# Kernel optimization log

Hardware: AMD Instinct MI355X
Metric: run time of the kernel (lower is better)

Reference implementation:

```python
import jax, jax.numpy as jnp
import numpy as np

TAU = 0.9
TOPK = 8
NUM_LAYERS = 3


def _layer_norm(x, g, b, eps=1e-5):
    mu = jnp.mean(x, axis=-1, keepdims=True)
    var = jnp.var(x, axis=-1, keepdims=True)
    return (x - mu) / jnp.sqrt(var + eps) * g + b


def _forward(x, edge_index, Wi, bi, wp, Wa, ba, ln1_g, ln1_b, ln2_g, ln2_b,
             W1, b1, W2, b2, Wc, bc, Wo, bo):
    N = x.shape[0]
    H = Wi.shape[1]
    # input projection + relu
    x = jax.nn.relu(x @ Wi + bi)
    src, dst = edge_index[0], edge_index[1]
    # ---- priority pi (computed under no_grad, dummy_alpha = 1, x_prev = 0) ----
    delta_x = jnp.sum(jnp.abs(x), axis=1)                      # [N]
    neigh = jax.ops.segment_sum(delta_x[src], dst, num_segments=N)
    pi = jax.lax.stop_gradient(jax.nn.sigmoid(x @ wp + neigh))  # [N]
    # ---- add self loops (selected subgraph == full graph) ----
    loops = jnp.arange(N, dtype=src.dtype)
    src_e = jnp.concatenate([src, loops])
    dst_e = jnp.concatenate([dst, loops])
    Et = src_e.shape[0]
    # ---- edge attention logits: att_mlp(cat[h_i, h_j, p_j]) computed as split matvec ----
    a_dst = x @ Wa[:H]          # contribution of h_i = x[dst]
    a_src = x @ Wa[H:2 * H]     # contribution of h_j = x[src]
    e = a_dst[dst_e] + a_src[src_e] + pi[src_e] * Wa[2 * H] + ba[0]
    e = jax.nn.leaky_relu(e, 0.2) / TAU
    e = jnp.clip(e, -5.0, 5.0)
    exp_e = jnp.exp(e)
    denom = jax.ops.segment_sum(exp_e, dst_e, num_segments=N)
    alpha = exp_e / (denom[dst_e] + 1e-16)
    # ---- per-destination top-k sparsification + renormalization (vectorized) ----
    order = jnp.lexsort((-alpha, dst_e))       # sort by dst, then alpha descending
    dst_s = dst_e[order]
    alpha_s = alpha[order]
    pos = jnp.arange(Et)
    is_new = jnp.concatenate([jnp.ones((1,), bool), dst_s[1:] != dst_s[:-1]])
    grp_start = jax.lax.cummax(jnp.where(is_new, pos, 0))
    rank = pos - grp_start                     # rank within each dst group
    keep = rank < TOPK
    ksum = jax.ops.segment_sum(jnp.where(keep, alpha_s, 0.0), dst_s, num_segments=N)
    alpha_new_s = jnp.where(keep, alpha_s / (ksum[dst_s] + 1e-16), 0.0)
    alpha = jnp.zeros((Et,), x.dtype).at[order].set(alpha_new_s)
    # ---- prenorm blocks with priority-weighted conv (dropout = identity, eval) ----
    h = x
    for l in range(NUM_LAYERS):
        hn = _layer_norm(h, ln1_g[l], ln1_b[l])
        xp = hn @ Wc[l] + bc[l]                               # conv linear
        msg = xp[src_e] * alpha[:, None]                      # [Et, H]
        agg = jax.ops.segment_sum(msg, dst_e, num_segments=N)  # scatter-add
        h = h + jax.nn.relu(agg)
        h2 = _layer_norm(h, ln2_g[l], ln2_b[l])
        h2 = jax.nn.gelu(h2 @ W1[l] + b1[l], approximate=False) @ W2[l] + b2[l]
        h = h + h2
    return h @ Wo + bo


def setup_inputs() -> dict:
    key = jax.random.key(0)
    ks = jax.random.split(key, 10)
    N, E, IN, H, OUT, L, F = 50000, 400000, 256, 256, 64, 3, 512
    def nrm(k, shape, scale):
        return jax.random.normal(k, shape, jnp.float32) * scale
    return {
        "x": nrm(ks[0], (N, IN), 1.0),
        "edge_index": jax.random.randint(ks[1], (2, E), 0, N, dtype=jnp.int32),
        "Wi": nrm(ks[2], (IN, H), IN ** -0.5), "bi": jnp.zeros((H,), jnp.float32),
        "wp": nrm(ks[3], (H,), H ** -0.5),
        "Wa": nrm(ks[4], (2 * H + 1,), (2 * H + 1) ** -0.5), "ba": jnp.zeros((1,), jnp.float32),
        "ln1_g": jnp.ones((L, H), jnp.float32), "ln1_b": jnp.zeros((L, H), jnp.float32),
        "ln2_g": jnp.ones((L, H), jnp.float32), "ln2_b": jnp.zeros((L, H), jnp.float32),
        "W1": nrm(ks[5], (L, H, F), H ** -0.5), "b1": jnp.zeros((L, F), jnp.float32),
        "W2": nrm(ks[6], (L, F, H), F ** -0.5), "b2": jnp.zeros((L, H), jnp.float32),
        "Wc": nrm(ks[7], (L, H, H), H ** -0.5), "bc": jnp.zeros((L, H), jnp.float32),
        "Wo": nrm(ks[8], (H, OUT), H ** -0.5), "bo": jnp.zeros((OUT,), jnp.float32),
    }


def reference(x, edge_index, Wi, bi, wp, Wa, ba, ln1_g, ln1_b, ln2_g, ln2_b,
              W1, b1, W2, b2, Wc, bc, Wo, bo):
    return _forward(x, edge_index, Wi, bi, wp, Wa, ba, ln1_g, ln1_b, ln2_g, ln2_b,
                    W1, b1, W2, b2, Wc, bc, Wo, bo)
```

## Files before the change

kernel.cpp:

```cpp
#include <hip/hip_runtime.h>
#include <math.h>

#define TAUF 0.9f

typedef unsigned int u32;
typedef unsigned short ushort;
typedef __attribute__((ext_vector_type(8))) short short8;
typedef __attribute__((ext_vector_type(8))) _Float16 half8;
typedef __attribute__((ext_vector_type(4))) float f32x4;
typedef __attribute__((ext_vector_type(4))) unsigned short us4;
typedef __attribute__((ext_vector_type(8))) unsigned short us8;

__device__ __forceinline__ ushort f2bf(float f) {
  u32 u = __builtin_bit_cast(u32, f);
  u32 r = (u + 0x7FFFu + ((u >> 16) & 1u)) >> 16;
  return (ushort)r;
}
__device__ __forceinline__ float bf2f(ushort s) {
  u32 u = ((u32)s) << 16;
  return __builtin_bit_cast(float, u);
}

__device__ __forceinline__ float gelu_f(float x) {
  float z = x * 0.70710678118654752f;
  float az = fabsf(z);
  float t = 1.f / fmaf(0.3275911f, az, 1.f);
  float poly = t * fmaf(t, fmaf(t, fmaf(t, fmaf(t, 1.061405429f, -1.453152027f),
                                        1.421413741f), -0.284496736f), 0.254829592f);
  float erfa = fmaf(-poly, __expf(-az * az), 1.f);
  float s = (z < 0.f) ? -erfa : erfa;
  return 0.5f * x * (1.f + s);
}

__device__ __forceinline__ void gload16(const void* g, void* l) {
  __builtin_amdgcn_global_load_lds(
      (const __attribute__((address_space(1))) u32*)g,
      (__attribute__((address_space(3))) u32*)l, 16, 0, 0);
}

__launch_bounds__(256, 2)
__global__ void gemm_in_mfma(const float* __restrict__ X,
                             const _Float16* __restrict__ Bh, const _Float16* __restrict__ Bl,
                             const float* __restrict__ bias, const float* __restrict__ Wa,
                             const float* __restrict__ wp, const float* __restrict__ g1,
                             const float* __restrict__ b1g, float* __restrict__ C,
                             ushort* __restrict__ hn, float* __restrict__ delta,
                             float* __restrict__ adst, float* __restrict__ asrc,
                             float* __restrict__ xwp, int M) {
  __shared__ char lds[40960];
  char* As_h = lds;
  char* As_l = lds + 4096;
  char* Bs_h = lds + 8192;
  char* Bs_l = lds + 24576;
  const int tid = threadIdx.x;
  const int wave = tid >> 6, lane = tid & 63;
  const int bm = blockIdx.x * 64;

  const int arow = tid >> 2;
  const int achunk = tid & 3;
  const int abyte = arow * 64 + ((achunk ^ ((arow >> 1) & 3)) << 4);
  const int brow = lane >> 2;
  const int bcol = (((lane & 3) ^ ((lane >> 3) & 3)) << 3);

  f32x4 accH[4][4], accC[4][4];
#pragma unroll
  for (int i = 0; i < 4; ++i)
#pragma unroll
    for (int j = 0; j < 4; ++j) {
      accH[i][j] = (f32x4){0.f, 0.f, 0.f, 0.f};
      accC[i][j] = (f32x4){0.f, 0.f, 0.f, 0.f};
    }

  int ar = bm + arow;
  ar = (ar < M) ? ar : (M - 1);
  const float* xrow = X + (size_t)ar * 256 + achunk * 8;

  for (int k0 = 0; k0 < 256; k0 += 32) {
    float4 x0 = *reinterpret_cast<const float4*>(xrow + k0);
    float4 x1 = *reinterpret_cast<const float4*>(xrow + k0 + 4);
    float xs[8] = {x0.x, x0.y, x0.z, x0.w, x1.x, x1.y, x1.z, x1.w};
    half8 hh, ll;
#pragma unroll
    for (int j = 0; j < 8; ++j) {
      _Float16 hv = (_Float16)xs[j];
      hh[j] = hv;
      ll[j] = (_Float16)((xs[j] - (float)hv) * 2048.f);
    }
    *reinterpret_cast<half8*>(As_h + abyte) = hh;
    *reinterpret_cast<half8*>(As_l + abyte) = ll;
#pragma unroll
    for (int r = 0; r < 4; ++r) {
      const int ch = r * 4 + wave;
      const int br = ch * 16 + brow;
      gload16(Bh + (size_t)br * 256 + k0 + bcol, Bs_h + ch * 1024);
      gload16(Bl + (size_t)br * 256 + k0 + bcol, Bs_l + ch * 1024);
    }
    __syncthreads();
    const int fs = lane >> 4;
    half8 ah[4], al[4];
#pragma unroll
    for (int mi = 0; mi < 4; ++mi) {
      const int rr = mi * 16 + (lane & 15);
      const int off = rr * 64 + ((fs ^ ((rr >> 1) & 3)) << 4);
      ah[mi] = *(const half8*)(As_h + off);
      al[mi] = *(const half8*)(As_l + off);
    }
#pragma unroll
    for (int ni = 0; ni < 4; ++ni) {
      const int rr = wave * 64 + ni * 16 + (lane & 15);
      half8 bh = *(const half8*)(Bs_h + rr * 64 + ((fs ^ ((rr >> 1) & 3)) << 4));
#pragma unroll
      for (int mi = 0; mi < 4; ++mi)
        accH[mi][ni] = __builtin_amdgcn_mfma_f32_16x16x32_f16(ah[mi], bh,
                                                              accH[mi][ni], 0, 0, 0);
#pragma unroll
      for (int mi = 0; mi < 4; ++mi)
        accC[mi][ni] = __builtin_amdgcn_mfma_f32_16x16x32_f16(al[mi], bh,
                                                              accC[mi][ni], 0, 0, 0);
    }
#pragma unroll
    for (int ni = 0; ni < 4; ++ni) {
      const int rr = wave * 64 + ni * 16 + (lane & 15);
      half8 bl = *(const half8*)(Bs_l + rr * 64 + ((fs ^ ((rr >> 1) & 3)) << 4));
#pragma unroll
      for (int mi = 0; mi < 4; ++mi)
        accC[mi][ni] = __builtin_amdgcn_mfma_f32_16x16x32_f16(ah[mi], bl,
                                                              accC[mi][ni], 0, 0, 0);
    }
    __syncthreads();
  }

  float bb[4], wa0[4], wa1[4], wpv[4], gg[4], gb[4];
#pragma unroll
  for (int ni = 0; ni < 4; ++ni) {
    const int c = wave * 64 + ni * 16 + (lane & 15);
    bb[ni] = bias[c]; wa0[ni] = Wa[c]; wa1[ni] = Wa[256 + c];
    wpv[ni] = wp[c]; gg[ni] = g1[c]; gb[ni] = b1g[c];
  }
  float* red = (float*)lds;
  float* muA = (float*)(lds + 5120);
  float* isA = (float*)(lds + 5376);
  const float inv = 1.f / 2048.f;
#pragma unroll
  for (int mi = 0; mi < 4; ++mi) {
#pragma unroll
    for (int reg = 0; reg < 4; ++reg) {
      const int lrow = mi * 16 + (lane >> 4) * 4 + reg;
      const int row = bm + lrow;
      float v[4];
      float p0 = 0.f, p1 = 0.f, p2 = 0.f, p3 = 0.f, p4 = 0.f;
#pragma unroll
      for (int ni = 0; ni < 4; ++ni) {
        float t = accH[mi][ni][reg] + accC[mi][ni][reg] * inv + bb[ni];
        t = fmaxf(t, 0.f);
        v[ni] = t;
        p0 += t; p1 += t * wa0[ni]; p2 += t * wa1[ni]; p3 += t * wpv[ni];
        p4 += t * t;
      }
      if (row < M) {
#pragma unroll
        for (int ni = 0; ni < 4; ++ni)
          C[(size_t)row * 256 + wave * 64 + ni * 16 + (lane & 15)] = v[ni];
      }
#pragma unroll
      for (int ni = 0; ni < 4; ++ni) accH[mi][ni][reg] = v[ni];
#pragma unroll
      for (int off = 1; off < 16; off <<= 1) {
        p0 += __shfl_xor(p0, off, 64);
        p1 += __shfl_xor(p1, off, 64);
        p2 += __shfl_xor(p2, off, 64);
        p3 += __shfl_xor(p3, off, 64);
        p4 += __shfl_xor(p4, off, 64);
      }
      if ((lane & 15) == 0) {
        red[(0 * 4 + wave) * 64 + lrow] = p0;
        red[(1 * 4 + wave) * 64 + lrow] = p1;
        red[(2 * 4 + wave) * 64 + lrow] = p2;
        red[(3 * 4 + wave) * 64 + lrow] = p3;
        red[(4 * 4 + wave) * 64 + lrow] = p4;
      }
    }
  }
  __syncthreads();
  if (tid < 64) {
    float s0 = 0.f, s1 = 0.f, s2 = 0.f, s3 = 0.f, s4 = 0.f;
#pragma unroll
    for (int w = 0; w < 4; ++w) {
      s0 += red[(0 * 4 + w) * 64 + tid];
      s1 += red[(1 * 4 + w) * 64 + tid];
      s2 += red[(2 * 4 + w) * 64 + tid];
      s3 += red[(3 * 4 + w) * 64 + tid];
      s4 += red[(4 * 4 + w) * 64 + tid];
    }
    const int row = bm + tid;
    if (row < M) {
      delta[row] = s0; adst[row] = s1; asrc[row] = s2; xwp[row] = s3;
    }
    float mu = s0 * (1.f / 256.f);
    muA[tid] = mu;
    isA[tid] = rsqrtf(s4 * (1.f / 256.f) - mu * mu + 1e-5f);
  }
  __syncthreads();
#pragma unroll
  for (int mi = 0; mi < 4; ++mi) {
#pragma unroll
    for (int reg = 0; reg < 4; ++reg) {
      const int lrow = mi * 16 + (lane >> 4) * 4 + reg;
      const int row = bm + lrow;
      if (row >= M) continue;
      const float mu = muA[lrow], is = isA[lrow];
#pragma unroll
      for (int ni = 0; ni < 4; ++ni) {
        const int col = wave * 64 + ni * 16 + (lane & 15);
        hn[(size_t)row * 256 + col] = f2bf((accH[mi][ni][reg] - mu) * is * gg[ni] + gb[ni]);
      }
    }
  }
}

__global__ void gather_k(const ushort* __restrict__ hn, const int* __restrict__ ksrc,
                         const float* __restrict__ kw, ushort* __restrict__ hagg, int N) {
  int d = blockIdx.x * 8 + (threadIdx.x >> 5);
  if (d >= N) return;
  int sub = threadIdx.x & 31;
  us8 xv[8];
  float w[8];
#pragma unroll
  for (int j = 0; j < 8; ++j) {
    int s = ksrc[(size_t)d * 8 + j];
    w[j] = kw[(size_t)d * 8 + j];
    xv[j] = *reinterpret_cast<const us8*>(hn + (size_t)s * 256 + sub * 8);
  }
  float a[8] = {0.f, 0.f, 0.f, 0.f, 0.f, 0.f, 0.f, 0.f};
#pragma unroll
  for (int j = 0; j < 8; ++j)
#pragma unroll
    for (int q = 0; q < 8; ++q) a[q] += w[j] * bf2f(xv[j][q]);
  us8 o;
#pragma unroll
  for (int q = 0; q < 8; ++q) o[q] = f2bf(a[q]);
  *reinterpret_cast<us8*>(hagg + (size_t)d * 256 + sub * 8) = o;
}

__launch_bounds__(512, 4)
__global__ void gemm_conv_aggln(const ushort* __restrict__ A, const ushort* __restrict__ Bt,
                                const float* __restrict__ bias, const float* __restrict__ g2,
                                const float* __restrict__ b2g, float* __restrict__ h,
                                ushort* __restrict__ hn, int M) {
  __shared__ ushort As[128 * 64];
  __shared__ ushort Bs[256 * 64];
  const int tid = threadIdx.x;
  const int wave = tid >> 6, lane = tid & 63;
  const int bm = blockIdx.x * 128;
  const int wm = (wave >> 2) * 64, wn = (wave & 3) * 64;
  const int srow = lane >> 3;
  const int scol = (((lane & 7) ^ srow) << 3);

  f32x4 acc[4][4];
#pragma unroll
  for (int i = 0; i < 4; ++i)
#pragma unroll
    for (int j = 0; j < 4; ++j) acc[i][j] = (f32x4){0.f, 0.f, 0.f, 0.f};

  for (int k0 = 0; k0 < 256; k0 += 64) {
#pragma unroll
    for (int r = 0; r < 2; ++r) {
      const int ch = r * 8 + wave;
      int ar = bm + ch * 8 + srow;
      ar = (ar < M) ? ar : (M - 1);
      gload16(A + (size_t)ar * 256 + k0 + scol, (char*)As + ch * 1024);
    }
#pragma unroll
    for (int r = 0; r < 4; ++r) {
      const int ch = r * 8 + wave;
      const int br = ch * 8 + srow;
      gload16(Bt + (size_t)br * 256 + k0 + scol, (char*)Bs + ch * 1024);
    }
    __syncthreads();
#pragma unroll
    for (int kk = 0; kk < 2; ++kk) {
      const int c = (kk * 32 + (lane >> 4) * 8) * 2;
      short8 a[4];
#pragma unroll
      for (int mi = 0; mi < 4; ++mi) {
        const int rr = wm + mi * 16 + (lane & 15);
        a[mi] = *(const short8*)((const char*)As + rr * 128 + (c ^ ((rr & 7) << 4)));
      }
#pragma unroll
      for (int ni = 0; ni < 4; ++ni) {
        const int rr = wn + ni * 16 + (lane & 15);
        short8 b = *(const short8*)((const char*)Bs + rr * 128 + (c ^ ((rr & 7) << 4)));
#pragma unroll
        for (int mi = 0; mi < 4; ++mi)
          acc[mi][ni] = __builtin_amdgcn_mfma_f32_16x16x32_bf16(a[mi], b,
                                                                acc[mi][ni], 0, 0, 0);
      }
    }
    __syncthreads();
  }

  float bb[4];
#pragma unroll
  for (int ni = 0; ni < 4; ++ni) bb[ni] = bias[wn + ni * 16 + (lane & 15)];

  float* redS = (float*)As;
  float* redQ = redS + 512;
  float* muA  = redQ + 512;
  float* isA  = muA + 128;

#pragma unroll
  for (int mi = 0; mi < 4; ++mi) {
#pragma unroll
    for (int reg = 0; reg < 4; ++reg) {
      const int lrow = wm + mi * 16 + (lane >> 4) * 4 + reg;
      const int row = bm + lrow;
      const bool ok = (row < M);
      float pS = 0.f, pQ = 0.f;
#pragma unroll
      for (int ni = 0; ni < 4; ++ni) {
        const int col = wn + ni * 16 + (lane & 15);
        float t = fmaxf(acc[mi][ni][reg] + bb[ni], 0.f);
        if (ok) {
          t += h[(size_t)row * 256 + col];
          h[(size_t)row * 256 + col] = t;
        }
        acc[mi][ni][reg] = t;
        pS += t;
        pQ += t * t;
      }
#pragma unroll
      for (int off = 1; off < 16; off <<= 1) {
        pS += __shfl_xor(pS, off, 64);
        pQ += __shfl_xor(pQ, off, 64);
      }
      if ((lane & 15) == 0) {
        redS[(wave & 3) * 128 + lrow] = pS;
        redQ[(wave & 3) * 128 + lrow] = pQ;
      }
    }
  }
  __syncthreads();
  if (tid < 128) {
    float S = redS[tid] + redS[128 + tid] + redS[256 + tid] + redS[384 + tid];
    float Q = redQ[tid] + redQ[128 + tid] + redQ[256 + tid] + redQ[384 + tid];
    float mu = S * (1.f / 256.f);
    muA[tid] = mu;
    isA[tid] = rsqrtf(Q * (1.f / 256.f) - mu * mu + 1e-5f);
  }
  __syncthreads();
  float gg[4], gb[4];
#pragma unroll
  for (int ni = 0; ni < 4; ++ni) {
    gg[ni] = g2[wn + ni * 16 + (lane & 15)];
    gb[ni] = b2g[wn + ni * 16 + (lane & 15)];
  }
#pragma unroll
  for (int mi = 0; mi < 4; ++mi) {
#pragma unroll
    for (int reg = 0; reg < 4; ++reg) {
      const int lrow = wm + mi * 16 + (lane >> 4) * 4 + reg;
      const int row = bm + lrow;
      if (row >= M) continue;
      const float mu = muA[lrow], is = isA[lrow];
#pragma unroll
      for (int ni = 0; ni < 4; ++ni) {
        const int col = wn + ni * 16 + (lane & 15);
        hn[(size_t)row * 256 + col] = f2bf((acc[mi][ni][reg] - mu) * is * gg[ni] + gb[ni]);
      }
    }
  }
}

__launch_bounds__(512, 4)
__global__ void gemm_ffn1(const ushort* __restrict__ A, const ushort* __restrict__ Bt,
                          const float* __restrict__ bias, ushort* __restrict__ u, int M) {
  __shared__ ushort As[128 * 64];
  __shared__ ushort Bs[256 * 64];
  const int tid = threadIdx.x;
  const int wave = tid >> 6, lane = tid & 63;
  const int bm = blockIdx.x * 128;
  const int bn = blockIdx.y * 256;
  const int wm = (wave >> 2) * 64, wn = (wave & 3) * 64;
  const int srow = lane >> 3;
  const int scol = (((lane & 7) ^ srow) << 3);

  f32x4 acc[4][4];
#pragma unroll
  for (int i = 0; i < 4; ++i)
#pragma unroll
    for (int j = 0; j < 4; ++j) acc[i][j] = (f32x4){0.f, 0.f, 0.f, 0.f};

  for (int k0 = 0; k0 < 256; k0 += 64) {
#pragma unroll
    for (int r = 0; r < 2; ++r) {
      const int ch = r * 8 + wave;
      int ar = bm + ch * 8 + srow;
      ar = (ar < M) ? ar : (M - 1);
      gload16(A + (size_t)ar * 256 + k0 + scol, (char*)As + ch * 1024);
    }
#pragma unroll
    for (int r = 0; r < 4; ++r) {
      const int ch = r * 8 + wave;
      const int br = bn + ch * 8 + srow;
      gload16(Bt + (size_t)br * 256 + k0 + scol, (char*)Bs + ch * 1024);
    }
    __syncthreads();
#pragma unroll
    for (int kk = 0; kk < 2; ++kk) {
      const int c = (kk * 32 + (lane >> 4) * 8) * 2;
      short8 a[4];
#pragma unroll
      for (int mi = 0; mi < 4; ++mi) {
        const int rr = wm + mi * 16 + (lane & 15);
        a[mi] = *(const short8*)((const char*)As + rr * 128 + (c ^ ((rr & 7) << 4)));
      }
#pragma unroll
      for (int ni = 0; ni < 4; ++ni) {
        const int rr = wn + ni * 16 + (lane & 15);
        short8 b = *(const short8*)((const char*)Bs + rr * 128 + (c ^ ((rr & 7) << 4)));
#pragma unroll
        for (int mi = 0; mi < 4; ++mi)
          acc[mi][ni] = __builtin_amdgcn_mfma_f32_16x16x32_bf16(a[mi], b,
                                                                acc[mi][ni], 0, 0, 0);
      }
    }
    __syncthreads();
  }

  float bb[4];
#pragma unroll
  for (int ni = 0; ni < 4; ++ni) bb[ni] = bias[bn + wn + ni * 16 + (lane & 15)];
#pragma unroll
  for (int mi = 0; mi < 4; ++mi) {
#pragma unroll
    for (int reg = 0; reg < 4; ++reg) {
      const int row = bm + wm + mi * 16 + (lane >> 4) * 4 + reg;
      if (row >= M) continue;
#pragma unroll
      for (int ni = 0; ni < 4; ++ni) {
        const int col = bn + wn + ni * 16 + (lane & 15);
        u[(size_t)row * 512 + col] = f2bf(gelu_f(acc[mi][ni][reg] + bb[ni]));
      }
    }
  }
}

template <int LAST>
__launch_bounds__(512, 4)
__global__ void gemm_ffn2ln(const ushort* __restrict__ A, const ushort* __restrict__ Bt,
                            const float* __restrict__ bias, const float* __restrict__ g1,
                            const float* __restrict__ b1g, float* __restrict__ h,
                            ushort* __restrict__ hn, int M) {
  __shared__ ushort As[128 * 64];
  __shared__ ushort Bs[256 * 64];
  const int tid = threadIdx.x;
  const int wave = tid >> 6, lane = tid & 63;
  const int bm = blockIdx.x * 128;
  const int wm = (wave >> 2) * 64, wn = (wave & 3) * 64;
  const int srow = lane >> 3;
  const int scol = (((lane & 7) ^ srow) << 3);

  f32x4 acc[4][4];
#pragma unroll
  for (int i = 0; i < 4; ++i)
#pragma unroll
    for (int j = 0; j < 4; ++j) acc[i][j] = (f32x4){0.f, 0.f, 0.f, 0.f};

  for (int k0 = 0; k0 < 512; k0 += 64) {
#pragma unroll
    for (int r = 0; r < 2; ++r) {
      const int ch = r * 8 + wave;
      int ar = bm + ch * 8 + srow;
      ar = (ar < M) ? ar : (M - 1);
      gload16(A + (size_t)ar * 512 + k0 + scol, (char*)As + ch * 1024);
    }
#pragma unroll
    for (int r = 0; r < 4; ++r) {
      const int ch = r * 8 + wave;
      const int br = ch * 8 + srow;
      gload16(Bt + (size_t)br * 512 + k0 + scol, (char*)Bs + ch * 1024);
    }
    __syncthreads();
#pragma unroll
    for (int kk = 0; kk < 2; ++kk) {
      const int c = (kk * 32 + (lane >> 4) * 8) * 2;
      short8 a[4];
#pragma unroll
      for (int mi = 0; mi < 4; ++mi) {
        const int rr = wm + mi * 16 + (lane & 15);
        a[mi] = *(const short8*)((const char*)As + rr * 128 + (c ^ ((rr & 7) << 4)));
      }
#pragma unroll
      for (int ni = 0; ni < 4; ++ni) {
        const int rr = wn + ni * 16 + (lane & 15);
        short8 b = *(const short8*)((const char*)Bs + rr * 128 + (c ^ ((rr & 7) << 4)));
#pragma unroll
        for (int mi = 0; mi < 4; ++mi)
          acc[mi][ni] = __builtin_amdgcn_mfma_f32_16x16x32_bf16(a[mi], b,
                                                                acc[mi][ni], 0, 0, 0);
      }
    }
    __syncthreads();
  }

  float bb[4];
#pragma unroll
  for (int ni = 0; ni < 4; ++ni) bb[ni] = bias[wn + ni * 16 + (lane & 15)];

  float* redS = (float*)As;
  float* redQ = redS + 512;
  float* muA  = redQ + 512;
  float* isA  = muA + 128;

#pragma unroll
  for (int mi = 0; mi < 4; ++mi) {
#pragma unroll
    for (int reg = 0; reg < 4; ++reg) {
      const int lrow = wm + mi * 16 + (lane >> 4) * 4 + reg;
      const int row = bm + lrow;
      const bool ok = (row < M);
      float pS = 0.f, pQ = 0.f;
#pragma unroll
      for (int ni = 0; ni < 4; ++ni) {
        const int col = wn + ni * 16 + (lane & 15);
        float t = acc[mi][ni][reg] + bb[ni];
        if (ok) t += h[(size_t)row * 256 + col];
        acc[mi][ni][reg] = t;
        if (LAST) {
          if (ok) hn[(size_t)row * 256 + col] = f2bf(t);
        } else {
          if (ok) h[(size_t)row * 256 + col] = t;
          pS += t;
          pQ += t * t;
        }
      }
      if (!LAST) {
#pragma unroll
        for (int off = 1; off < 16; off <<= 1) {
          pS += __shfl_xor(pS, off, 64);
          pQ += __shfl_xor(pQ, off, 64);
        }
        if ((lane & 15) == 0) {
          redS[(wave & 3) * 128 + lrow] = pS;
          redQ[(wave & 3) * 128 + lrow] = pQ;
        }
      }
    }
  }
  if (LAST) return;
  __syncthreads();
  if (tid < 128) {
    float S = redS[tid] + redS[128 + tid] + redS[256 + tid] + redS[384 + tid];
    float Q = redQ[tid] + redQ[128 + tid] + redQ[256 + tid] + redQ[384 + tid];
    float mu = S * (1.f / 256.f);
    muA[tid] = mu;
    isA[tid] = rsqrtf(Q * (1.f / 256.f) - mu * mu + 1e-5f);
  }
  __syncthreads();
  float gg[4], gb[4];
#pragma unroll
  for (int ni = 0; ni < 4; ++ni) {
    gg[ni] = g1[wn + ni * 16 + (lane & 15)];
    gb[ni] = b1g[wn + ni * 16 + (lane & 15)];
  }
#pragma unroll
  for (int mi = 0; mi < 4; ++mi) {
#pragma unroll
    for (int reg = 0; reg < 4; ++reg) {
      const int lrow = wm + mi * 16 + (lane >> 4) * 4 + reg;
      const int row = bm + lrow;
      if (row >= M) continue;
      const float mu = muA[lrow], is = isA[lrow];
#pragma unroll
      for (int ni = 0; ni < 4; ++ni) {
        const int col = wn + ni * 16 + (lane & 15);
        hn[(size_t)row * 256 + col] = f2bf((acc[mi][ni][reg] - mu) * is * gg[ni] + gb[ni]);
      }
    }
  }
}

__launch_bounds__(256)
__global__ void gemm_out(const ushort* __restrict__ A, const ushort* __restrict__ Bt,
                         const float* __restrict__ bias, float* __restrict__ C, int M) {
  __shared__ ushort As[128 * 64];
  __shared__ ushort Bs[64 * 64];
  const int tid = threadIdx.x;
  const int wave = tid >> 6, lane = tid & 63;
  const int bm = blockIdx.x * 128;
  const int wm = wave * 32;
  const int srow = lane >> 3;
  const int scol = (((lane & 7) ^ srow) << 3);
  f32x4 acc[2][4];
#pragma unroll
  for (int i = 0; i < 2; ++i)
#pragma unroll
    for (int j = 0; j < 4; ++j) acc[i][j] = (f32x4){0.f, 0.f, 0.f, 0.f};

  for (int k0 = 0; k0 < 256; k0 += 64) {
#pragma unroll
    for (int r = 0; r < 4; ++r) {
      const int ch = r * 4 + wave;
      int ar = bm + ch * 8 + srow;
      ar = (ar < M) ? ar : (M - 1);
      gload16(A + (size_t)ar * 256 + k0 + scol, (char*)As + ch * 1024);
    }
#pragma unroll
    for (int r = 0; r < 2; ++r) {
      const int ch = r * 4 + wave;
      const int br = ch * 8 + srow;
      gload16(Bt + (size_t)br * 256 + k0 + scol, (char*)Bs + ch * 1024);
    }
    __syncthreads();
#pragma unroll
    for (int kk = 0; kk < 2; ++kk) {
      const int c = (kk * 32 + (lane >> 4) * 8) * 2;
      short8 a[2], b[4];
#pragma unroll
      for (int mi = 0; mi < 2; ++mi) {
        const int rr = wm + mi * 16 + (lane & 15);
        a[mi] = *(const short8*)((const char*)As + rr * 128 + (c ^ ((rr & 7) << 4)));
      }
#pragma unroll
      for (int ni = 0; ni < 4; ++ni) {
        const int rr = ni * 16 + (lane & 15);
        b[ni] = *(const short8*)((const char*)Bs + rr * 128 + (c ^ ((rr & 7) << 4)));
      }
#pragma unroll
      for (int mi = 0; mi < 2; ++mi)
#pragma unroll
        for (int ni = 0; ni < 4; ++ni)
          acc[mi][ni] = __builtin_amdgcn_mfma_f32_16x16x32_bf16(a[mi], b[ni],
                                                                acc[mi][ni], 0, 0, 0);
    }
    __syncthreads();
  }
  float bb[4];
#pragma unroll
  for (int ni = 0; ni < 4; ++ni) bb[ni] = bias[ni * 16 + (lane & 15)];
#pragma unroll
  for (int mi = 0; mi < 2; ++mi) {
#pragma unroll
    for (int reg = 0; reg < 4; ++reg) {
      const int row = bm + wm + mi * 16 + (lane >> 4) * 4 + reg;
      if (row >= M) continue;
#pragma unroll
      for (int ni = 0; ni < 4; ++ni) {
        const int col = ni * 16 + (lane & 15);
        C[(size_t)row * 64 + col] = acc[mi][ni][reg] + bb[ni];
      }
    }
  }
}

#define W_IN 65536
#define W_TOTAL (196608 + 393216 + 393216 + 16384)
__global__ void prep_k(const float* __restrict__ Wi, const float* __restrict__ Wc,
                       const float* __restrict__ W1, const float* __restrict__ W2,
                       const float* __restrict__ Wo, _Float16* __restrict__ WiTh,
                       _Float16* __restrict__ WiTl, ushort* __restrict__ WcT,
                       ushort* __restrict__ W1T, ushort* __restrict__ W2T,
                       ushort* __restrict__ WoT, float* __restrict__ zbase, int zn) {
  int i = blockIdx.x * 256 + threadIdx.x;
  if (i < W_IN) {
    int n = i >> 8, k = i & 255;
    float w = Wi[(size_t)k * 256 + n];
    _Float16 hv = (_Float16)w;
    WiTh[i] = hv;
    WiTl[i] = (_Float16)((w - (float)hv) * 2048.f);
  } else if ((i -= W_IN) < W_TOTAL) {
    int j = i;
    if (j < 196608) {
      int l = j / 65536, r = j % 65536, n = r >> 8, k = r & 255;
      WcT[j] = f2bf(Wc[(size_t)l * 65536 + k * 256 + n]);
    } else if ((j -= 196608) < 393216) {
      int l = j / 131072, r = j % 131072, n = r >> 8, k = r & 255;
      W1T[j] = f2bf(W1[(size_t)l * 131072 + k * 512 + n]);
    } else if ((j -= 393216) < 393216) {
      int l = j / 131072, r = j % 131072, n = r >> 9, k = r & 511;
      W2T[j] = f2bf(W2[(size_t)l * 131072 + k * 256 + n]);
    } else {
      j -= 393216;
      int n = j >> 8, k = j & 255;
      WoT[j] = f2bf(Wo[k * 64 + n]);
    }
  } else {
    int z = i - W_TOTAL;
    if (z < zn) zbase[z] = 0.f;
  }
}

__global__ void neigh_k(const int* __restrict__ src, const int* __restrict__ dst,
                        const float* __restrict__ delta, float* __restrict__ neigh, int E) {
  int e = blockIdx.x * 256 + threadIdx.x;
  if (e < E) atomicAdd(&neigh[dst[e]], delta[src[e]]);
}

__global__ void logits_k(const int* __restrict__ src, const int* __restrict__ dst,
                         const float* __restrict__ adst, const float* __restrict__ asrc,
                         const float* __restrict__ xwp, const float* __restrict__ neigh,
                         const float* __restrict__ Wa, const float* __restrict__ ba,
                         float* __restrict__ expe, float* __restrict__ denom,
                         int* __restrict__ cnt, int* __restrict__ slots,
                         int E, int Et, int N) {
  int e = blockIdx.x * 256 + threadIdx.x;
  if (e >= Et) return;
  int s, d;
  if (e < E) { s = src[e]; d = dst[e]; } else { s = e - E; d = s; }
  float pis = 1.f / (1.f + expf(-(xwp[s] + neigh[s])));
  float v = adst[d] + asrc[s] + pis * Wa[512] + ba[0];
  v = (v >= 0.f ? v : 0.2f * v) / TAUF;
  v = fminf(fmaxf(v, -5.f), 5.f);
  float ex = expf(v);
  expe[e] = ex;
  atomicAdd(&denom[d], ex);
  int p = atomicAdd(&cnt[d], 1);
  if (p < 64) slots[(size_t)p * N + d] = e;
}

__device__ __forceinline__ bool better(float a, int e, float a2, int e2) {
  return a > a2 || (a == a2 && e < e2);
}

__global__ void topk_k(const int* __restrict__ cnt, const int* __restrict__ slots,
                       const float* __restrict__ expe, const float* __restrict__ denom,
                       const int* __restrict__ src, int* __restrict__ ksrc,
                       float* __restrict__ kw, int N, int E) {
  int d = blockIdx.x * 256 + threadIdx.x;
  if (d >= N) return;
  int deg = min(cnt[d], 64);
  float D = denom[d] + 1e-16f;
  float av[8]; int ai[8]; int kc = 0;
  for (int t = 0; t < deg; ++t) {
    int e = slots[(size_t)t * N + d];
    float a = expe[e] / D;
    if (kc < 8) {
      int p = kc++;
      while (p > 0 && better(a, e, av[p - 1], ai[p - 1])) {
        av[p] = av[p - 1]; ai[p] = ai[p - 1]; --p;
      }
      av[p] = a; ai[p] = e;
    } else if (better(a, e, av[7], ai[7])) {
      int p = 7;
      while (p > 0 && better(a, e, av[p - 1], ai[p - 1])) {
        av[p] = av[p - 1]; ai[p] = ai[p - 1]; --p;
      }
      av[p] = a; ai[p] = e;
    }
  }
  float ks = 0.f;
  for (int j = 0; j < kc; ++j) ks += av[j];
  float inv = 1.f / (ks + 1e-16f);
#pragma unroll
  for (int j = 0; j < 8; ++j) {
    if (j < kc) {
      int e = ai[j];
      ksrc[(size_t)d * 8 + j] = (e < E) ? src[e] : (e - E);
      kw[(size_t)d * 8 + j] = av[j] * inv;
    } else {
      ksrc[(size_t)d * 8 + j] = 0;
      kw[(size_t)d * 8 + j] = 0.f;
    }
  }
}

extern "C" void kernel_launch(void* const* d_in, const int* in_sizes, int n_in,
                              void* d_out, int out_size, void* d_ws, size_t ws_size,
                              hipStream_t stream) {
  const float* X   = (const float*)d_in[0];
  const int*   EI  = (const int*)d_in[1];
  const float* Wi  = (const float*)d_in[2];
  const float* bi  = (const float*)d_in[3];
  const float* wp  = (const float*)d_in[4];
  const float* Wa  = (const float*)d_in[5];
  const float* ba  = (const float*)d_in[6];
  const float* l1g = (const float*)d_in[7];
  const float* l1b = (const float*)d_in[8];
  const float* l2g = (const float*)d_in[9];
  const float* l2b = (const float*)d_in[10];
  const float* W1  = (const float*)d_in[11];
  const float* b1  = (const float*)d_in[12];
  const float* W2  = (const float*)d_in[13];
  const float* b2  = (const float*)d_in[14];
  const float* Wc  = (const float*)d_in[15];
  const float* bc  = (const float*)d_in[16];
  const float* Wo  = (const float*)d_in[17];
  const float* bo  = (const float*)d_in[18];

  const int N = in_sizes[0] / 256;
  const int E = in_sizes[1] / 2;
  const int Et = E + N;
  const int* srcp = EI;
  const int* dstp = EI + E;

  float* ws = (float*)d_ws;
  size_t off = 0;
  auto alloc = [&](size_t n) { float* p = ws + off; off += n; return p; };
  const size_t NH = (size_t)N * 256;
  float*  h    = alloc(NH);
  ushort* hn   = (ushort*)alloc(NH / 2);
  ushort* hagg = (ushort*)alloc(NH / 2);
  ushort* u    = (ushort*)alloc(NH);
  _Float16* WiTh = (_Float16*)alloc(65536 / 2);
  _Float16* WiTl = (_Float16*)alloc(65536 / 2);
  ushort* WcT  = (ushort*)alloc(3 * 65536 / 2);
  ushort* W1T  = (ushort*)alloc(3 * 131072 / 2);
  ushort* W2T  = (ushort*)alloc(3 * 131072 / 2);
  ushort* WoT  = (ushort*)alloc(16384 / 2);
  float* delta = alloc(N);
  float* adst  = alloc(N);
  float* asrc  = alloc(N);
  float* xwp   = alloc(N);
  float* expe  = alloc(Et);
  float* neigh = alloc(N);
  float* denom = alloc(N);
  int*   cnt   = (int*)alloc(N);
  int*   slots = (int*)alloc((size_t)N * 64);
  int*   ksrc  = (int*)alloc((size_t)N * 8);
  float* kw    = alloc((size_t)N * 8);

  prep_k<<<(W_IN + W_TOTAL + 3 * N + 255) / 256, 256, 0, stream>>>(
      Wi, Wc, W1, W2, Wo, WiTh, WiTl, WcT, W1T, W2T, WoT, neigh, 3 * N);

  gemm_in_mfma<<<(N + 63) / 64, 256, 0, stream>>>(
      X, WiTh, WiTl, bi, Wa, wp, l1g, l1b, h, hn,
      delta, adst, asrc, xwp, N);
  neigh_k<<<(E + 255) / 256, 256, 0, stream>>>(srcp, dstp, delta, neigh, E);
  logits_k<<<(Et + 255) / 256, 256, 0, stream>>>(srcp, dstp, adst, asrc, xwp, neigh,
                                                 Wa, ba, expe, denom, cnt, slots,
                                                 E, Et, N);
  topk_k<<<(N + 255) / 256, 256, 0, stream>>>(cnt, slots, expe, denom, srcp,
                                              ksrc, kw, N, E);

  const int GM = (N + 127) / 128;
  for (int l = 0; l < 3; ++l) {
    gather_k<<<(N + 7) / 8, 256, 0, stream>>>(hn, ksrc, kw, hagg, N);
    gemm_conv_aggln<<<GM, 512, 0, stream>>>(
        hagg, WcT + (size_t)l * 65536, bc + l * 256,
        l2g + l * 256, l2b + l * 256, h, hn, N);
    gemm_ffn1<<<dim3(GM, 2), 512, 0, stream>>>(
        hn, W1T + (size_t)l * 131072, b1 + l * 512, u, N);
    if (l < 2)
      gemm_ffn2ln<0><<<GM, 512, 0, stream>>>(
          u, W2T + (size_t)l * 131072, b2 + l * 256,
          l1g + (l + 1) * 256, l1b + (l + 1) * 256, h, hn, N);
    else
      gemm_ffn2ln<1><<<GM, 512, 0, stream>>>(
          u, W2T + (size_t)l * 131072, b2 + l * 256,
          nullptr, nullptr, h, hn, N);
  }
  gemm_out<<<(N + 127) / 128, 256, 0, stream>>>(hn, WoT, bo, (float*)d_out, N);
}
```

Measured before the change: 636.6 us.

## Fuse top-k neighbor gather into conv GEMM prologue; widen input GEMM K-tile

The separate gather kernel is removed. The conv GEMM now gathers and weights the 8 top-k neighbor rows of hn directly into registers, then stages them into shared memory for each K slice. This removes the hagg round trip through global memory and one launch per layer. The cost is more registers (launch bounds lowered to 2 blocks) and gather latency inside the GEMM. A ping-pong buffer hn2 avoids the read-write hazard on hn. Separately, the input GEMM uses K-steps of 64 with a matching 128-byte swizzle, doubling LDS to 80KB and halving barrier count.

```diff
diff --git a/kernel.cpp b/kernel.cpp
--- a/kernel.cpp
+++ b/kernel.cpp
@@ -47,20 +47,21 @@
                              ushort* __restrict__ hn, float* __restrict__ delta,
                              float* __restrict__ adst, float* __restrict__ asrc,
                              float* __restrict__ xwp, int M) {
-  __shared__ char lds[40960];
+  __shared__ char lds[81920];
   char* As_h = lds;
-  char* As_l = lds + 4096;
-  char* Bs_h = lds + 8192;
-  char* Bs_l = lds + 24576;
+  char* As_l = lds + 8192;
+  char* Bs_h = lds + 16384;
+  char* Bs_l = lds + 49152;
   const int tid = threadIdx.x;
   const int wave = tid >> 6, lane = tid & 63;
   const int bm = blockIdx.x * 64;
 
   const int arow = tid >> 2;
-  const int achunk = tid & 3;
-  const int abyte = arow * 64 + ((achunk ^ ((arow >> 1) & 3)) << 4);
-  const int brow = lane >> 2;
-  const int bcol = (((lane & 3) ^ ((lane >> 3) & 3)) << 3);
+  const int ac4 = tid & 3;
+  const int aoff0 = arow * 128 + (((2 * ac4 + 0) ^ (arow & 7)) << 4);
+  const int aoff1 = arow * 128 + (((2 * ac4 + 1) ^ (arow & 7)) << 4);
+  const int srow = lane >> 3;
+  const int scol = (((lane & 7) ^ srow) << 3);
 
   f32x4 accH[4][4], accC[4][4];
 #pragma unroll
@@ -73,59 +74,71 @@
 
   int ar = bm + arow;
   ar = (ar < M) ? ar : (M - 1);
-  const float* xrow = X + (size_t)ar * 256 + achunk * 8;
-
-  for (int k0 = 0; k0 < 256; k0 += 32) {
+  const float* xrow = X + (size_t)ar * 256 + ac4 * 16;
+
+#pragma unroll
+  for (int k0 = 0; k0 < 256; k0 += 64) {
     float4 x0 = *reinterpret_cast<const float4*>(xrow + k0);
     float4 x1 = *reinterpret_cast<const float4*>(xrow + k0 + 4);
-    float xs[8] = {x0.x, x0.y, x0.z, x0.w, x1.x, x1.y, x1.z, x1.w};
-    half8 hh, ll;
+    float4 x2 = *reinterpret_cast<const float4*>(xrow + k0 + 8);
+    float4 x3 = *reinterpret_cast<const float4*>(xrow + k0 + 12);
+    float xs[16] = {x0.x, x0.y, x0.z, x0.w, x1.x, x1.y, x1.z, x1.w,
+                    x2.x, x2.y, x2.z, x2.w, x3.x, x3.y, x3.z, x3.w};
+    half8 hh0, hh1, ll0, ll1;
 #pragma unroll
     for (int j = 0; j < 8; ++j) {
       _Float16 hv = (_Float16)xs[j];
-      hh[j] = hv;
-      ll[j] = (_Float16)((xs[j] - (float)hv) * 2048.f);
-    }
-    *reinterpret_cast<half8*>(As_h + abyte) = hh;
-    *reinterpret_cast<half8*>(As_l + abyte) = ll;
-#pragma unroll
-    for (int r = 0; r < 4; ++r) {
+      hh0[j] = hv;
+      ll0[j] = (_Float16)((xs[j] - (float)hv) * 2048.f);
+      _Float16 hv2 = (_Float16)xs[8 + j];
+      hh1[j] = hv2;
+      ll1[j] = (_Float16)((xs[8 + j] - (float)hv2) * 2048.f);
+    }
+    *reinterpret_cast<half8*>(As_h + aoff0) = hh0;
+    *reinterpret_cast<half8*>(As_h + aoff1) = hh1;
+    *reinterpret_cast<half8*>(As_l + aoff0) = ll0;
+    *reinterpret_cast<half8*>(As_l + aoff1) = ll1;
+#pragma unroll
+    for (int r = 0; r < 8; ++r) {
       const int ch = r * 4 + wave;
-      const int br = ch * 16 + brow;
-      gload16(Bh + (size_t)br * 256 + k0 + bcol, Bs_h + ch * 1024);
-      gload16(Bl + (size_t)br * 256 + k0 + bcol, Bs_l + ch * 1024);
-    }
-    __syncthreads();
-    const int fs = lane >> 4;
-    half8 ah[4], al[4];
-#pragma unroll
-    for (int mi = 0; mi < 4; ++mi) {
-      const int rr = mi * 16 + (lane & 15);
-      const int off = rr * 64 + ((fs ^ ((rr >> 1) & 3)) << 4);
-      ah[mi] = *(const half8*)(As_h + off);
-      al[mi] = *(const half8*)(As_l + off);
-    }
-#pragma unroll
-    for (int ni = 0; ni < 4; ++ni) {
-      const int rr = wave * 64 + ni * 16 + (lane & 15);
-      half8 bh = *(const half8*)(Bs_h + rr * 64 + ((fs ^ ((rr >> 1) & 3)) << 4));
-#pragma unroll
-      for (int mi = 0; mi < 4; ++mi)
-        accH[mi][ni] = __builtin_amdgcn_mfma_f32_16x16x32_f16(ah[mi], bh,
-                                                              accH[mi][ni], 0, 0, 0);
-#pragma unroll
-      for (int mi = 0; mi < 4; ++mi)
-        accC[mi][ni] = __builtin_amdgcn_mfma_f32_16x16x32_f16(al[mi], bh,
-                                                              accC[mi][ni], 0, 0, 0);
-    }
-#pragma unroll
-    for (int ni = 0; ni < 4; ++ni) {
-      const int rr = wave * 64 + ni * 16 + (lane & 15);
-      half8 bl = *(const half8*)(Bs_l + rr * 64 + ((fs ^ ((rr >> 1) & 3)) << 4));
-#pragma unroll
-      for (int mi = 0; mi < 4; ++mi)
-        accC[mi][ni] = __builtin_amdgcn_mfma_f32_16x16x32_f16(ah[mi], bl,
-                                                              accC[mi][ni], 0, 0, 0);
+      const int br = ch * 8 + srow;
+      gload16(Bh + (size_t)br * 256 + k0 + scol, Bs_h + ch * 1024);
+      gload16(Bl + (size_t)br * 256 + k0 + scol, Bs_l + ch * 1024);
+    }
+    __syncthreads();
+#pragma unroll
+    for (int kk = 0; kk < 2; ++kk) {
+      const int c = (kk * 32 + (lane >> 4) * 8) * 2;
+      half8 ah[4], al[4];
+#pragma unroll
+      for (int mi = 0; mi < 4; ++mi) {
+        const int rr = mi * 16 + (lane & 15);
+        const int off = rr * 128 + (c ^ ((rr & 7) << 4));
+        ah[mi] = *(const half8*)(As_h + off);
+        al[mi] = *(const half8*)(As_l + off);
+      }
+#pragma unroll
+      for (int ni = 0; ni < 4; ++ni) {
+        const int rr = wave * 64 + ni * 16 + (lane & 15);
+        half8 bh = *(const half8*)(Bs_h + rr * 128 + (c ^ ((rr & 7) << 4)));
+#pragma unroll
+        for (int mi = 0; mi < 4; ++mi)
+          accH[mi][ni] = __builtin_amdgcn_mfma_f32_16x16x32_f16(ah[mi], bh,
+                                                                accH[mi][ni], 0, 0, 0);
+#pragma unroll
+        for (int mi = 0; mi < 4; ++mi)
+          accC[mi][ni] = __builtin_amdgcn_mfma_f32_16x16x32_f16(al[mi], bh,
+                                                                accC[mi][ni], 0, 0, 0);
+      }
+#pragma unroll
+      for (int ni = 0; ni < 4; ++ni) {
+        const int rr = wave * 64 + ni * 16 + (lane & 15);
+        half8 bl = *(const half8*)(Bs_l + rr * 128 + (c ^ ((rr & 7) << 4)));
+#pragma unroll
+        for (int mi = 0; mi < 4; ++mi)
+          accC[mi][ni] = __builtin_amdgcn_mfma_f32_16x16x32_f16(ah[mi], bl,
+                                                                accC[mi][ni], 0, 0, 0);
+      }
     }
     __syncthreads();
   }
@@ -218,35 +231,12 @@
   }
 }
 
-__global__ void gather_k(const ushort* __restrict__ hn, const int* __restrict__ ksrc,
-                         const float* __restrict__ kw, ushort* __restrict__ hagg, int N) {
-  int d = blockIdx.x * 8 + (threadIdx.x >> 5);
-  if (d >= N) return;
-  int sub = threadIdx.x & 31;
-  us8 xv[8];
-  float w[8];
-#pragma unroll
-  for (int j = 0; j < 8; ++j) {
-    int s = ksrc[(size_t)d * 8 + j];
-    w[j] = kw[(size_t)d * 8 + j];
-    xv[j] = *reinterpret_cast<const us8*>(hn + (size_t)s * 256 + sub * 8);
-  }
-  float a[8] = {0.f, 0.f, 0.f, 0.f, 0.f, 0.f, 0.f, 0.f};
-#pragma unroll
-  for (int j = 0; j < 8; ++j)
-#pragma unroll
-    for (int q = 0; q < 8; ++q) a[q] += w[j] * bf2f(xv[j][q]);
-  us8 o;
-#pragma unroll
-  for (int q = 0; q < 8; ++q) o[q] = f2bf(a[q]);
-  *reinterpret_cast<us8*>(hagg + (size_t)d * 256 + sub * 8) = o;
-}
-
-__launch_bounds__(512, 4)
-__global__ void gemm_conv_aggln(const ushort* __restrict__ A, const ushort* __restrict__ Bt,
-                                const float* __restrict__ bias, const float* __restrict__ g2,
-                                const float* __restrict__ b2g, float* __restrict__ h,
-                                ushort* __restrict__ hn, int M) {
+__launch_bounds__(512, 2)
+__global__ void gemm_conv_aggln(const ushort* __restrict__ hn_in,
+                                const int* __restrict__ ksrc, const float* __restrict__ kw,
+                                const ushort* __restrict__ Bt, const float* __restrict__ bias,
+                                const float* __restrict__ g2, const float* __restrict__ b2g,
+                                float* __restrict__ h, ushort* __restrict__ hn2, int M) {
   __shared__ ushort As[128 * 64];
   __shared__ ushort Bs[256 * 64];
   const int tid = threadIdx.x;
@@ -256,20 +246,55 @@
   const int srow = lane >> 3;
   const int scol = (((lane & 7) ^ srow) << 3);
 
+  const int arow = tid >> 2;
+  const int c4 = tid & 3;
+  int grow = bm + arow;
+  grow = (grow < M) ? grow : (M - 1);
+  int sidx[8];
+  float sw[8];
+#pragma unroll
+  for (int j = 0; j < 8; ++j) {
+    sidx[j] = ksrc[(size_t)grow * 8 + j];
+    sw[j] = kw[(size_t)grow * 8 + j];
+  }
+  us8 agg[4][2];
+#pragma unroll
+  for (int k = 0; k < 4; ++k) {
+    const int cb = k * 64 + c4 * 16;
+    float a[16];
+#pragma unroll
+    for (int q = 0; q < 16; ++q) a[q] = 0.f;
+#pragma unroll
+    for (int j = 0; j < 8; ++j) {
+      const ushort* p = hn_in + (size_t)sidx[j] * 256 + cb;
+      us8 v0 = *reinterpret_cast<const us8*>(p);
+      us8 v1 = *reinterpret_cast<const us8*>(p + 8);
+#pragma unroll
+      for (int q = 0; q < 8; ++q) {
+        a[q] += sw[j] * bf2f(v0[q]);
+        a[8 + q] += sw[j] * bf2f(v1[q]);
+      }
+    }
+    us8 o0, o1;
+#pragma unroll
+    for (int q = 0; q < 8; ++q) { o0[q] = f2bf(a[q]); o1[q] = f2bf(a[8 + q]); }
+    agg[k][0] = o0;
+    agg[k][1] = o1;
+  }
+  const int aoff0 = arow * 128 + (((2 * c4 + 0) ^ (arow & 7)) << 4);
+  const int aoff1 = arow * 128 + (((2 * c4 + 1) ^ (arow & 7)) << 4);
+
   f32x4 acc[4][4];
 #pragma unroll
   for (int i = 0; i < 4; ++i)
 #pragma unroll
     for (int j = 0; j < 4; ++j) acc[i][j] = (f32x4){0.f, 0.f, 0.f, 0.f};
 
-  for (int k0 = 0; k0 < 256; k0 += 64) {
-#pragma unroll
-    for (int r = 0; r < 2; ++r) {
-      const int ch = r * 8 + wave;
-      int ar = bm + ch * 8 + srow;
-      ar = (ar < M) ? ar : (M - 1);
-      gload16(A + (size_t)ar * 256 + k0 + scol, (char*)As + ch * 1024);
-    }
+#pragma unroll
+  for (int ks = 0; ks < 4; ++ks) {
+    const int k0 = ks * 64;
+    *reinterpret_cast<us8*>((char*)As + aoff0) = agg[ks][0];
+    *reinterpret_cast<us8*>((char*)As + aoff1) = agg[ks][1];
 #pragma unroll
     for (int r = 0; r < 4; ++r) {
       const int ch = r * 8 + wave;
@@ -280,11 +305,11 @@
 #pragma unroll
     for (int kk = 0; kk < 2; ++kk) {
       const int c = (kk * 32 + (lane >> 4) * 8) * 2;
-      short8 a[4];
+      short8 a4[4];
 #pragma unroll
       for (int mi = 0; mi < 4; ++mi) {
         const int rr = wm + mi * 16 + (lane & 15);
-        a[mi] = *(const short8*)((const char*)As + rr * 128 + (c ^ ((rr & 7) << 4)));
+        a4[mi] = *(const short8*)((const char*)As + rr * 128 + (c ^ ((rr & 7) << 4)));
       }
 #pragma unroll
       for (int ni = 0; ni < 4; ++ni) {
@@ -292,7 +317,7 @@
         short8 b = *(const short8*)((const char*)Bs + rr * 128 + (c ^ ((rr & 7) << 4)));
 #pragma unroll
         for (int mi = 0; mi < 4; ++mi)
-          acc[mi][ni] = __builtin_amdgcn_mfma_f32_16x16x32_bf16(a[mi], b,
+          acc[mi][ni] = __builtin_amdgcn_mfma_f32_16x16x32_bf16(a4[mi], b,
                                                                 acc[mi][ni], 0, 0, 0);
       }
     }
@@ -365,7 +390,7 @@
 #pragma unroll
       for (int ni = 0; ni < 4; ++ni) {
         const int col = wn + ni * 16 + (lane & 15);
-        hn[(size_t)row * 256 + col] = f2bf((acc[mi][ni][reg] - mu) * is * gg[ni] + gb[ni]);
+        hn2[(size_t)row * 256 + col] = f2bf((acc[mi][ni][reg] - mu) * is * gg[ni] + gb[ni]);
       }
     }
   }
@@ -799,7 +824,7 @@
   const size_t NH = (size_t)N * 256;
   float*  h    = alloc(NH);
   ushort* hn   = (ushort*)alloc(NH / 2);
-  ushort* hagg = (ushort*)alloc(NH / 2);
+  ushort* hn2  = (ushort*)alloc(NH / 2);
   ushort* u    = (ushort*)alloc(NH);
   _Float16* WiTh = (_Float16*)alloc(65536 / 2);
   _Float16* WiTl = (_Float16*)alloc(65536 / 2);
@@ -834,12 +859,11 @@
 
   const int GM = (N + 127) / 128;
   for (int l = 0; l < 3; ++l) {
-    gather_k<<<(N + 7) / 8, 256, 0, stream>>>(hn, ksrc, kw, hagg, N);
     gemm_conv_aggln<<<GM, 512, 0, stream>>>(
-        hagg, WcT + (size_t)l * 65536, bc + l * 256,
-        l2g + l * 256, l2b + l * 256, h, hn, N);
+        hn, ksrc, kw, WcT + (size_t)l * 65536, bc + l * 256,
+        l2g + l * 256, l2b + l * 256, h, hn2, N);
     gemm_ffn1<<<dim3(GM, 2), 512, 0, stream>>>(
-        hn, W1T + (size_t)l * 131072, b1 + l * 512, u, N);
+        hn2, W1T + (size_t)l * 131072, b1 + l * 512, u, N);
     if (l < 2)
       gemm_ffn2ln<0><<<GM, 512, 0, stream>>>(
           u, W2T + (size_t)l * 131072, b2 + l * 256,
```

New measurement: 675.3 us. 6.1% more time.
